# Kernel tuning notes

Hardware: AMD Instinct MI355X
Metric: run time of the kernel (lower is better)

The kernel has to match this reference:

```python
import jax, jax.numpy as jnp
import numpy as np

N_NODES = 50000
N_EDGES = 800000
F_IN = 128
HEADS = 4
C_OUT = 32
NEG_SLOPE = 0.2
BN_EPS = 1e-5


def _add_self_loops(edge_index, edge_attr, n):
    # PyG fill_value='mean': self-loop attr = mean of incoming edge attrs per node (0 if none)
    src, dst = edge_index[0], edge_index[1]
    deg = jax.ops.segment_sum(jnp.ones_like(edge_attr[:, 0]), dst, num_segments=n)
    loop_attr = jax.ops.segment_sum(edge_attr, dst, num_segments=n) / jnp.maximum(deg, 1.0)[:, None]
    loop = jnp.arange(n)
    src2 = jnp.concatenate([src, loop])
    dst2 = jnp.concatenate([dst, loop])
    attr2 = jnp.concatenate([edge_attr, loop_attr], axis=0)
    return src2, dst2, attr2


def _segment_softmax(logits, seg, n):
    m = jax.ops.segment_max(logits, seg, num_segments=n)
    m = jnp.where(jnp.isfinite(m), m, 0.0)
    ex = jnp.exp(logits - m[seg])
    s = jax.ops.segment_sum(ex, seg, num_segments=n)
    return ex / s[seg]


def _gatv2(x, src, dst, eattr, Wl, bl, Wr, br, We, att, bias, n):
    # x: [n, F]; returns [n, HEADS*C_OUT]
    xl = (x @ Wl + bl).reshape(n, HEADS, C_OUT)
    xr = (x @ Wr + br).reshape(n, HEADS, C_OUT)
    ea = (eattr @ We).reshape(-1, HEADS, C_OUT)
    xlj = xl[src]                                   # [E, H, C] gather
    msg = jax.nn.leaky_relu(xlj + xr[dst] + ea, NEG_SLOPE)
    logits = jnp.einsum('ehc,hc->eh', msg, att)     # [E, H]
    alpha = _segment_softmax(logits, dst, n)
    out = jax.ops.segment_sum(xlj * alpha[..., None], dst, num_segments=n)
    return out.reshape(n, HEADS * C_OUT) + bias


def _batchnorm(x, gamma, beta):
    mu = x.mean(axis=0)
    var = x.var(axis=0)
    return gamma * (x - mu) * jax.lax.rsqrt(var + BN_EPS) + beta


def setup_inputs() -> dict:
    key = jax.random.key(0)
    ks = jax.random.split(key, 20)
    HC = HEADS * C_OUT
    s = 0.05
    inp = {
        'emb': jax.random.normal(ks[0], (N_NODES, F_IN), dtype=jnp.float32),
        'edge_index': jax.random.randint(ks[1], (2, N_EDGES), 0, N_NODES, dtype=jnp.int64),
        'edge_weight': jax.random.uniform(ks[2], (N_EDGES, 1), dtype=jnp.float32),
        'Wl1': jax.random.normal(ks[3], (F_IN, HC)) * s,
        'bl1': jnp.zeros((HC,), jnp.float32),
        'Wr1': jax.random.normal(ks[4], (F_IN, HC)) * s,
        'br1': jnp.zeros((HC,), jnp.float32),
        'We1': jax.random.normal(ks[5], (1, HC)) * s,
        'att1': jax.random.normal(ks[6], (HEADS, C_OUT)) * s,
        'bias1': jnp.zeros((HC,), jnp.float32),
        'gamma1': jnp.ones((HC,), jnp.float32),
        'beta1': jnp.zeros((HC,), jnp.float32),
        'Wl2': jax.random.normal(ks[7], (HC, HC)) * s,
        'bl2': jnp.zeros((HC,), jnp.float32),
        'Wr2': jax.random.normal(ks[8], (HC, HC)) * s,
        'br2': jnp.zeros((HC,), jnp.float32),
        'We2': jax.random.normal(ks[9], (1, HC)) * s,
        'att2': jax.random.normal(ks[10], (HEADS, C_OUT)) * s,
        'bias2': jnp.zeros((HC,), jnp.float32),
    }
    return inp


def reference(emb, edge_index, edge_weight, Wl1, bl1, Wr1, br1, We1, att1, bias1,
              gamma1, beta1, Wl2, bl2, Wr2, br2, We2, att2, bias2):
    n = emb.shape[0]
    src, dst, eattr = _add_self_loops(edge_index, edge_weight, n)
    h1 = _gatv2(emb, src, dst, eattr, Wl1, bl1, Wr1, br1, We1, att1, bias1, n)
    h1 = jax.nn.elu(_batchnorm(h1, gamma1, beta1))
    h2 = _gatv2(h1, src, dst, eattr, Wl2, bl2, Wr2, br2, We2, att2, bias2, n)
    # fusion: mean over [input_emb, h1, h2] along stacked axis
    return (emb + h1 + h2) / 3.0
```

## Files before the change

kernel.cpp:

```cpp
#include <hip/hip_runtime.h>
#include <hip/hip_bf16.h>
#include <math.h>

#define N_NODES 50000
#define N_EDGES 800000
#define HC 128
#define SLOT 64

#define BM 128
#define NBX ((N_NODES + BM - 1) / BM)
#define NBKT 64
#define EPB (N_EDGES / NBKT)
#define NW (N_NODES / 2)

typedef short bh8 __attribute__((ext_vector_type(8)));
typedef float f4 __attribute__((ext_vector_type(4)));
typedef float f2 __attribute__((ext_vector_type(2)));

__device__ __forceinline__ unsigned int pk2(float a, float b) {
  return (unsigned int)__bfloat16_as_ushort(__float2bfloat16(a)) |
         ((unsigned int)__bfloat16_as_ushort(__float2bfloat16(b)) << 16);
}
__device__ __forceinline__ float blo(unsigned int u) { return __uint_as_float(u << 16); }
__device__ __forceinline__ float bhi(unsigned int u) { return __uint_as_float(u & 0xffff0000u); }

__global__ __launch_bounds__(256) void k_wprep(
    const float* __restrict__ Wl1, const float* __restrict__ Wr1,
    const float* __restrict__ Wl2, const float* __restrict__ Wr2,
    unsigned short* __restrict__ WtAll,
    float* __restrict__ chsum, float* __restrict__ chsq) {
  int gid = blockIdx.x * 256 + threadIdx.x;
  int m = gid >> 14;
  int idx = gid & 16383;
  const float* src = (m == 0) ? Wl1 : (m == 1) ? Wr1 : (m == 2) ? Wl2 : Wr2;
  int k = idx >> 7, n = idx & 127;
  WtAll[((size_t)m * HC + n) * HC + k] =
      __bfloat16_as_ushort(__float2bfloat16(src[k * HC + n]));
  if (gid < HC) { chsum[gid] = 0.f; chsq[gid] = 0.f; }
}

__global__ __launch_bounds__(1024) void k_hist(const int* __restrict__ ei,
                                               unsigned int* __restrict__ counts32) {
  __shared__ unsigned int hist[NW];
  int tid = threadIdx.x, b = blockIdx.x;
  for (int w = tid; w < NW; w += 1024) hist[w] = 0u;
  __syncthreads();
  const int* dstp = ei + N_EDGES + b * EPB;
  for (int g = tid; g < EPB / 4; g += 1024) {
    int4 d4 = *(const int4*)(dstp + g * 4);
    atomicAdd(&hist[d4.x >> 1], (d4.x & 1) ? 0x10000u : 1u);
    atomicAdd(&hist[d4.y >> 1], (d4.y & 1) ? 0x10000u : 1u);
    atomicAdd(&hist[d4.z >> 1], (d4.z & 1) ? 0x10000u : 1u);
    atomicAdd(&hist[d4.w >> 1], (d4.w & 1) ? 0x10000u : 1u);
  }
  __syncthreads();
  unsigned int* dst = counts32 + (size_t)b * NW;
  for (int w = tid; w < NW; w += 1024) dst[w] = hist[w];
}

__global__ __launch_bounds__(256) void k_scan(const unsigned int* __restrict__ counts32,
                                              unsigned int* __restrict__ bases32,
                                              int* __restrict__ cursor) {
  int w = blockIdx.x * 256 + threadIdx.x;
  if (w >= NW) return;
  unsigned int a0 = 0, a1 = 0;
#pragma unroll 4
  for (int b = 0; b < NBKT; ++b) {
    unsigned int v = counts32[(size_t)b * NW + w];
    bases32[(size_t)b * NW + w] = a0 | (a1 << 16);
    a0 += v & 0xffffu;
    a1 += v >> 16;
  }
  cursor[2 * w] = (int)a0;
  cursor[2 * w + 1] = (int)a1;
}

__global__ __launch_bounds__(256) void k_scat_g1(
    const int* __restrict__ ei, const float* __restrict__ ew,
    const unsigned int* __restrict__ bases32, unsigned int* __restrict__ slots,
    const float* __restrict__ X, const unsigned short* __restrict__ Wt,
    const float* __restrict__ b0, const float* __restrict__ b1,
    unsigned short* __restrict__ Y0b, float* __restrict__ Y1) {
  __shared__ __align__(16) unsigned int lsbuf[NW];
  int tid = threadIdx.x, bid = blockIdx.x;
  if (bid < NBKT) {
    const unsigned int* bp = bases32 + (size_t)bid * NW;
    for (int w = tid; w < NW; w += 256) lsbuf[w] = bp[w];
    __syncthreads();
    const int* sp = ei + bid * EPB;
    const int* dp = ei + N_EDGES + bid * EPB;
    const float* wp = ew + bid * EPB;
    for (int g = tid; g < EPB / 4; g += 256) {
      int4 s4 = *(const int4*)(sp + g * 4);
      int4 d4 = *(const int4*)(dp + g * 4);
      float4 w4 = *(const float4*)(wp + g * 4);
      int ss[4] = {s4.x, s4.y, s4.z, s4.w};
      int dd[4] = {d4.x, d4.y, d4.z, d4.w};
      float ww[4] = {w4.x, w4.y, w4.z, w4.w};
#pragma unroll
      for (int i = 0; i < 4; ++i) {
        unsigned int old = atomicAdd(&lsbuf[dd[i] >> 1], (dd[i] & 1) ? 0x10000u : 1u);
        unsigned int pos = (dd[i] & 1) ? (old >> 16) : (old & 0xffffu);
        unsigned int wq = min((unsigned int)(ww[i] * 65536.f + 0.5f), 65535u);
        if (pos < SLOT)
          slots[(size_t)dd[i] * SLOT + pos] = ((unsigned int)ss[i] << 16) | wq;
      }
    }
    return;
  }
  unsigned short* Xls = (unsigned short*)lsbuf;
  unsigned short* Wls = Xls + 128 * 128;
  int row0 = (bid - NBKT) * BM;
  {
    int r = tid >> 1;
    int ks = (tid & 1) * 64;
    int gr = row0 + r;
    const float* xp = X + (size_t)gr * HC + ks;
    int sw = r & 15;
#pragma unroll
    for (int i = 0; i < 4; ++i) {
      float f[16];
      if (gr < N_NODES) {
        *(float4*)&f[0] = *(const float4*)(xp + i * 16);
        *(float4*)&f[4] = *(const float4*)(xp + i * 16 + 4);
        *(float4*)&f[8] = *(const float4*)(xp + i * 16 + 8);
        *(float4*)&f[12] = *(const float4*)(xp + i * 16 + 12);
      } else {
#pragma unroll
        for (int j = 0; j < 16; ++j) f[j] = 0.f;
      }
      int kg = (ks >> 3) + i * 2;
      *(uint4*)&Xls[r * 128 + ((kg ^ sw) * 8)] =
          make_uint4(pk2(f[0], f[1]), pk2(f[2], f[3]), pk2(f[4], f[5]), pk2(f[6], f[7]));
      *(uint4*)&Xls[r * 128 + (((kg + 1) ^ sw) * 8)] =
          make_uint4(pk2(f[8], f[9]), pk2(f[10], f[11]), pk2(f[12], f[13]), pk2(f[14], f[15]));
    }
  }
  int lane = tid & 63;
  int wv = tid >> 6;
  int lrow = lane & 15;
  int lq = lane >> 4;
  int rbase = wv * 32;
#pragma unroll
  for (int half = 0; half < 2; ++half) {
    if (half) __syncthreads();
    {
      int n = tid >> 1;
      int ks2 = (tid & 1) * 64;
      const unsigned short* wp = Wt + half * (HC * HC) + n * HC + ks2;
      int swn = n & 15;
#pragma unroll
      for (int g = 0; g < 8; ++g) {
        uint4 v = *(const uint4*)(wp + g * 8);
        int kg = (ks2 >> 3) + g;
        *(uint4*)&Wls[n * 128 + ((kg ^ swn) * 8)] = v;
      }
    }
    __syncthreads();
    f4 acc[2][8];
#pragma unroll
    for (int mt = 0; mt < 2; ++mt)
#pragma unroll
      for (int nt = 0; nt < 8; ++nt) acc[mt][nt] = (f4){0.f, 0.f, 0.f, 0.f};
#pragma unroll
    for (int kk = 0; kk < 4; ++kk) {
      int kg = kk * 4 + lq;
      bh8 a0 = *(const bh8*)&Xls[(rbase + lrow) * 128 + ((kg ^ lrow) * 8)];
      bh8 a1 = *(const bh8*)&Xls[(rbase + 16 + lrow) * 128 + ((kg ^ lrow) * 8)];
#pragma unroll
      for (int nt = 0; nt < 8; ++nt) {
        bh8 b = *(const bh8*)&Wls[(nt * 16 + lrow) * 128 + ((kg ^ lrow) * 8)];
        acc[0][nt] = __builtin_amdgcn_mfma_f32_16x16x32_bf16(a0, b, acc[0][nt], 0, 0, 0);
        acc[1][nt] = __builtin_amdgcn_mfma_f32_16x16x32_bf16(a1, b, acc[1][nt], 0, 0, 0);
      }
    }
    const float* bb = half ? b1 : b0;
    float bv[8];
#pragma unroll
    for (int nt = 0; nt < 8; ++nt) bv[nt] = bb[nt * 16 + lrow];
#pragma unroll
    for (int mt = 0; mt < 2; ++mt) {
#pragma unroll
      for (int rr = 0; rr < 4; ++rr) {
        int gr = row0 + rbase + mt * 16 + lq * 4 + rr;
        if (gr < N_NODES) {
          if (half == 0) {
#pragma unroll
            for (int nt = 0; nt < 8; ++nt)
              Y0b[(size_t)gr * HC + nt * 16 + lrow] =
                  __bfloat16_as_ushort(__float2bfloat16(acc[mt][nt][rr] + bv[nt]));
          } else {
#pragma unroll
            for (int nt = 0; nt < 8; ++nt)
              Y1[(size_t)gr * HC + nt * 16 + lrow] = acc[mt][nt][rr] + bv[nt];
          }
        }
      }
    }
  }
}

__global__ __launch_bounds__(256) void k_gemm2(
    const unsigned short* __restrict__ Xb, const unsigned short* __restrict__ Wt,
    const float* __restrict__ b0, const float* __restrict__ b1,
    unsigned char* __restrict__ Y0f8, float* __restrict__ Y1,
    const float* __restrict__ chsum, const float* __restrict__ chsq,
    const float* __restrict__ gamma, const float* __restrict__ beta) {
  __shared__ __align__(16) unsigned short Xls[128 * 128];
  __shared__ __align__(16) unsigned short Wls[128 * 128];
  __shared__ float ssc[HC], ssh[HC];
  int tid = threadIdx.x;
  if (tid < HC) {
    float mu = chsum[tid] * (1.f / N_NODES);
    float var = chsq[tid] * (1.f / N_NODES) - mu * mu;
    float sc = gamma[tid] * rsqrtf(var + 1e-5f);
    ssc[tid] = sc;
    ssh[tid] = beta[tid] - mu * sc;
  }
  __syncthreads();
  int row0 = blockIdx.x * BM;
  {
    int r = tid >> 1;
    int ks = (tid & 1) * 64;
    int gr = row0 + r;
    const unsigned short* xp = Xb + (size_t)gr * HC + ks;
    int sw = r & 15;
#pragma unroll
    for (int i = 0; i < 4; ++i) {
      float f[16];
      if (gr < N_NODES) {
        uint4 ua = *(const uint4*)(xp + i * 16);
        uint4 ub = *(const uint4*)(xp + i * 16 + 8);
        f[0] = blo(ua.x); f[1] = bhi(ua.x); f[2] = blo(ua.y); f[3] = bhi(ua.y);
        f[4] = blo(ua.z); f[5] = bhi(ua.z); f[6] = blo(ua.w); f[7] = bhi(ua.w);
        f[8] = blo(ub.x); f[9] = bhi(ub.x); f[10] = blo(ub.y); f[11] = bhi(ub.y);
        f[12] = blo(ub.z); f[13] = bhi(ub.z); f[14] = blo(ub.w); f[15] = bhi(ub.w);
      } else {
#pragma unroll
        for (int j = 0; j < 16; ++j) f[j] = 0.f;
      }
#pragma unroll
      for (int j = 0; j < 16; ++j) {
        float y = fmaf(f[j], ssc[ks + i * 16 + j], ssh[ks + i * 16 + j]);
        f[j] = (y > 0.f) ? y : (__expf(y) - 1.f);
      }
      int kg = (ks >> 3) + i * 2;
      *(uint4*)&Xls[r * 128 + ((kg ^ sw) * 8)] =
          make_uint4(pk2(f[0], f[1]), pk2(f[2], f[3]), pk2(f[4], f[5]), pk2(f[6], f[7]));
      *(uint4*)&Xls[r * 128 + (((kg + 1) ^ sw) * 8)] =
          make_uint4(pk2(f[8], f[9]), pk2(f[10], f[11]), pk2(f[12], f[13]), pk2(f[14], f[15]));
    }
  }
  int lane = tid & 63;
  int wv = tid >> 6;
  int lrow = lane & 15;
  int lq = lane >> 4;
  int rbase = wv * 32;
#pragma unroll
  for (int half = 0; half < 2; ++half) {
    if (half) __syncthreads();
    {
      int n = tid >> 1;
      int ks = (tid & 1) * 64;
      const unsigned short* wp = Wt + half * (HC * HC) + n * HC + ks;
      int swn = n & 15;
#pragma unroll
      for (int g = 0; g < 8; ++g) {
        uint4 v = *(const uint4*)(wp + g * 8);
        int kg = (ks >> 3) + g;
        *(uint4*)&Wls[n * 128 + ((kg ^ swn) * 8)] = v;
      }
    }
    __syncthreads();
    f4 acc[2][8];
#pragma unroll
    for (int mt = 0; mt < 2; ++mt)
#pragma unroll
      for (int nt = 0; nt < 8; ++nt) acc[mt][nt] = (f4){0.f, 0.f, 0.f, 0.f};
#pragma unroll
    for (int kk = 0; kk < 4; ++kk) {
      int kg = kk * 4 + lq;
      bh8 a0 = *(const bh8*)&Xls[(rbase + lrow) * 128 + ((kg ^ lrow) * 8)];
      bh8 a1 = *(const bh8*)&Xls[(rbase + 16 + lrow) * 128 + ((kg ^ lrow) * 8)];
#pragma unroll
      for (int nt = 0; nt < 8; ++nt) {
        bh8 b = *(const bh8*)&Wls[(nt * 16 + lrow) * 128 + ((kg ^ lrow) * 8)];
        acc[0][nt] = __builtin_amdgcn_mfma_f32_16x16x32_bf16(a0, b, acc[0][nt], 0, 0, 0);
        acc[1][nt] = __builtin_amdgcn_mfma_f32_16x16x32_bf16(a1, b, acc[1][nt], 0, 0, 0);
      }
    }
    const float* bb = half ? b1 : b0;
    float bv[8];
#pragma unroll
    for (int nt = 0; nt < 8; ++nt) bv[nt] = bb[nt * 16 + lrow];
#pragma unroll
    for (int mt = 0; mt < 2; ++mt) {
#pragma unroll
      for (int rr = 0; rr < 4; ++rr) {
        int gr = row0 + rbase + mt * 16 + lq * 4 + rr;
        if (gr < N_NODES) {
          if (half == 0) {
#pragma unroll
            for (int nt = 0; nt < 8; ++nt) {
              float v = acc[mt][nt][rr] + bv[nt];
              int p = __builtin_amdgcn_cvt_pk_fp8_f32(v, v, 0, false);
              Y0f8[(size_t)gr * HC + nt * 16 + lrow] = (unsigned char)(p & 0xff);
            }
          } else {
#pragma unroll
            for (int nt = 0; nt < 8; ++nt)
              Y1[(size_t)gr * HC + nt * 16 + lrow] = acc[mt][nt][rr] + bv[nt];
          }
        }
      }
    }
  }
}

template <int FINAL, int F8>
__global__ __launch_bounds__(256) void k_gat(
    const void* __restrict__ xlv, const float* __restrict__ xr,
    const int* __restrict__ cursor, const unsigned int* __restrict__ slots,
    const float* __restrict__ We, const float* __restrict__ att,
    const float* __restrict__ bias, void* __restrict__ out,
    const float* __restrict__ emb, const unsigned short* __restrict__ h1p,
    const float* __restrict__ chsum, const float* __restrict__ chsq,
    const float* __restrict__ gamma, const float* __restrict__ beta) {
  int g = threadIdx.x >> 5;
  int lane = threadIdx.x & 31;
  int n = blockIdx.x * 8 + g;
  int fi = n * 32 + lane;
  const uint2* xl2 = (const uint2*)xlv;
  const unsigned int* xf = (const unsigned int*)xlv;
  float4 xr4 = ((const float4*)xr)[fi];
  float4 we4 = ((const float4*)We)[lane];
  float4 at4 = ((const float4*)att)[lane];
  int deg = min(cursor[n], SLOT);
  int base = n * SLOT;
  int deg32 = min(deg, 32);

  unsigned int ev = (lane < deg32) ? slots[base + lane] : 0u;
  float evw = (float)(ev & 0xffffu) * (1.f / 65536.f);
  float wsum = evw;
#pragma unroll
  for (int m = 16; m >= 1; m >>= 1) wsum += __shfl_xor(wsum, m);

  float l = 0.f;
  float4 o = make_float4(0.f, 0.f, 0.f, 0.f);

  auto decode = [&](uint2 gc) -> float4 {
    float4 xlj;
    if (F8) {
      f2 ab = __builtin_amdgcn_cvt_pk_f32_fp8((int)gc.x, false);
      f2 cd = __builtin_amdgcn_cvt_pk_f32_fp8((int)gc.x, true);
      xlj.x = ab[0]; xlj.y = ab[1]; xlj.z = cd[0]; xlj.w = cd[1];
    } else {
      xlj.x = blo(gc.x); xlj.y = bhi(gc.x);
      xlj.z = blo(gc.y); xlj.w = bhi(gc.y);
    }
    return xlj;
  };
  auto edge_body = [&](float w, uint2 gc, bool valid) {
    float4 xlj = decode(gc);
    float4 v;
    v.x = fmaf(w, we4.x, xlj.x + xr4.x);
    v.y = fmaf(w, we4.y, xlj.y + xr4.y);
    v.z = fmaf(w, we4.z, xlj.z + xr4.z);
    v.w = fmaf(w, we4.w, xlj.w + xr4.w);
    v.x = fmaxf(v.x, 0.2f * v.x);
    v.y = fmaxf(v.y, 0.2f * v.y);
    v.z = fmaxf(v.z, 0.2f * v.z);
    v.w = fmaxf(v.w, 0.2f * v.w);
    float p = v.x * at4.x + v.y * at4.y + v.z * at4.z + v.w * at4.w;
    p += __shfl_xor(p, 1);
    p += __shfl_xor(p, 2);
    p += __shfl_xor(p, 4);
    float e = valid ? __expf(p) : 0.f;
    l += e;
    o.x = fmaf(e, xlj.x, o.x);
    o.y = fmaf(e, xlj.y, o.y);
    o.z = fmaf(e, xlj.z, o.z);
    o.w = fmaf(e, xlj.w, o.w);
  };
  auto fetch = [&](int j, uint2& qq, float& ww) {
    int jc = min(j, deg32 - 1);
    unsigned int evj = __shfl(ev, jc, 32);
    ww = (float)(evj & 0xffffu) * (1.f / 65536.f);
    int s = (int)(evj >> 16);
    if (F8) qq.x = xf[s * 32 + lane];
    else qq = xl2[s * 32 + lane];
  };

  if (deg32 > 0) {
    uint2 q0, q1, q2, q3;
    float w0, w1, w2, w3;
    fetch(0, q0, w0);
    fetch(1, q1, w1);
    fetch(2, q2, w2);
    fetch(3, q3, w3);
    for (int b = 0; b < deg32; b += 4) {
      uint2 c0 = q0, c1 = q1, c2 = q2, c3 = q3;
      float x0 = w0, x1 = w1, x2 = w2, x3 = w3;
      fetch(b + 4, q0, w0);
      fetch(b + 5, q1, w1);
      fetch(b + 6, q2, w2);
      fetch(b + 7, q3, w3);
      edge_body(x0, c0, true);
      edge_body(x1, c1, b + 1 < deg32);
      edge_body(x2, c2, b + 2 < deg32);
      edge_body(x3, c3, b + 3 < deg32);
    }
  }
  if (deg > 32) {
    for (int j = base + 32; j < base + deg; ++j) {
      unsigned int evj = slots[j];
      float w = (float)(evj & 0xffffu) * (1.f / 65536.f);
      wsum += w;
      int s = (int)(evj >> 16);
      uint2 gc;
      if (F8) gc.x = xf[s * 32 + lane];
      else gc = xl2[s * 32 + lane];
      edge_body(w, gc, true);
    }
  }
  {
    float wself = (deg > 0) ? wsum / (float)deg : 0.f;
    uint2 gs;
    if (F8) gs.x = xf[n * 32 + lane];
    else gs = xl2[n * 32 + lane];
    edge_body(wself, gs, true);
  }

  float inv = 1.f / l;
  float4 b4 = ((const float4*)bias)[lane];
  float4 r;
  r.x = fmaf(o.x, inv, b4.x);
  r.y = fmaf(o.y, inv, b4.y);
  r.z = fmaf(o.z, inv, b4.z);
  r.w = fmaf(o.w, inv, b4.w);
  if (FINAL) {
    float4 e4 = ((const float4*)emb)[fi];
    uint2 hh = ((const uint2*)h1p)[fi];
    float4 h4;
    h4.x = blo(hh.x); h4.y = bhi(hh.x); h4.z = blo(hh.y); h4.w = bhi(hh.y);
    float4 cs = ((const float4*)chsum)[lane];
    float4 cq = ((const float4*)chsq)[lane];
    float4 gm = ((const float4*)gamma)[lane];
    float4 bt = ((const float4*)beta)[lane];
    const float invN = 1.f / N_NODES;
    float4 sc4, sh4;
    {
      float mu = cs.x * invN, var = cq.x * invN - mu * mu;
      sc4.x = gm.x * rsqrtf(var + 1e-5f); sh4.x = bt.x - mu * sc4.x;
      mu = cs.y * invN; var = cq.y * invN - mu * mu;
      sc4.y = gm.y * rsqrtf(var + 1e-5f); sh4.y = bt.y - mu * sc4.y;
      mu = cs.z * invN; var = cq.z * invN - mu * mu;
      sc4.z = gm.z * rsqrtf(var + 1e-5f); sh4.z = bt.z - mu * sc4.z;
      mu = cs.w * invN; var = cq.w * invN - mu * mu;
      sc4.w = gm.w * rsqrtf(var + 1e-5f); sh4.w = bt.w - mu * sc4.w;
    }
    float4 h;
    h.x = fmaf(h4.x, sc4.x, sh4.x);
    h.y = fmaf(h4.y, sc4.y, sh4.y);
    h.z = fmaf(h4.z, sc4.z, sh4.z);
    h.w = fmaf(h4.w, sc4.w, sh4.w);
    h.x = (h.x > 0.f) ? h.x : (__expf(h.x) - 1.f);
    h.y = (h.y > 0.f) ? h.y : (__expf(h.y) - 1.f);
    h.z = (h.z > 0.f) ? h.z : (__expf(h.z) - 1.f);
    h.w = (h.w > 0.f) ? h.w : (__expf(h.w) - 1.f);
    const float k3 = 1.f / 3.f;
    r.x = (e4.x + h.x + r.x) * k3;
    r.y = (e4.y + h.y + r.y) * k3;
    r.z = (e4.z + h.z + r.z) * k3;
    r.w = (e4.w + h.w + r.w) * k3;
    ((float4*)out)[fi] = r;
  } else {
    ((uint2*)out)[fi] = make_uint2(pk2(r.x, r.y), pk2(r.z, r.w));
  }
}

#define BN_ROWS 200
__global__ __launch_bounds__(256) void k_bnstats(const unsigned short* __restrict__ h1b,
                                                 float* __restrict__ chsum,
                                                 float* __restrict__ chsq) {
  int c2 = threadIdx.x & 63;
  int g = threadIdx.x >> 6;
  int r0 = blockIdx.x * BN_ROWS;
  float s0 = 0.f, s1 = 0.f, q0 = 0.f, q1 = 0.f;
  const unsigned int* h32 = (const unsigned int*)h1b;
  for (int r = r0 + g; r < r0 + BN_ROWS; r += 4) {
    unsigned int u = h32[(size_t)r * 64 + c2];
    float a = blo(u), b = bhi(u);
    s0 += a; q0 += a * a;
    s1 += b; q1 += b * b;
  }
  __shared__ float sh[256][4];
  sh[threadIdx.x][0] = s0; sh[threadIdx.x][1] = q0;
  sh[threadIdx.x][2] = s1; sh[threadIdx.x][3] = q1;
  __syncthreads();
  if (g == 0) {
    float ts0 = 0.f, tq0 = 0.f, ts1 = 0.f, tq1 = 0.f;
#pragma unroll
    for (int gg = 0; gg < 4; ++gg) {
      ts0 += sh[gg * 64 + c2][0]; tq0 += sh[gg * 64 + c2][1];
      ts1 += sh[gg * 64 + c2][2]; tq1 += sh[gg * 64 + c2][3];
    }
    atomicAdd(chsum + 2 * c2, ts0);
    atomicAdd(chsq + 2 * c2, tq0);
    atomicAdd(chsum + 2 * c2 + 1, ts1);
    atomicAdd(chsq + 2 * c2 + 1, tq1);
  }
}

extern "C" void kernel_launch(void* const* d_in, const int* in_sizes, int n_in,
                              void* d_out, int out_size, void* d_ws, size_t ws_size,
                              hipStream_t stream) {
  const float* emb = (const float*)d_in[0];
  const int* ei = (const int*)d_in[1];
  const float* ew = (const float*)d_in[2];
  const float* Wl1 = (const float*)d_in[3];
  const float* bl1 = (const float*)d_in[4];
  const float* Wr1 = (const float*)d_in[5];
  const float* br1 = (const float*)d_in[6];
  const float* We1 = (const float*)d_in[7];
  const float* att1 = (const float*)d_in[8];
  const float* bias1 = (const float*)d_in[9];
  const float* gamma1 = (const float*)d_in[10];
  const float* beta1 = (const float*)d_in[11];
  const float* Wl2 = (const float*)d_in[12];
  const float* bl2 = (const float*)d_in[13];
  const float* Wr2 = (const float*)d_in[14];
  const float* br2 = (const float*)d_in[15];
  const float* We2 = (const float*)d_in[16];
  const float* att2 = (const float*)d_in[17];
  const float* bias2 = (const float*)d_in[18];
  float* out = (float*)d_out;

  char* wsb = (char*)d_ws;
  size_t off = 0;
  auto alloc = [&](size_t bytes) -> void* {
    void* p = (void*)(wsb + off);
    off += (bytes + 255) & ~(size_t)255;
    return p;
  };
  int* cursor = (int*)alloc((size_t)N_NODES * 4);
  float* chsum = (float*)alloc(HC * 4);
  float* chsq = (float*)alloc(HC * 4);
  unsigned short* WtAll = (unsigned short*)alloc((size_t)4 * HC * HC * 2);
  unsigned int* counts32 = (unsigned int*)alloc((size_t)NBKT * NW * 4);
  unsigned int* bases32 = (unsigned int*)alloc((size_t)NBKT * NW * 4);
  unsigned int* slots = (unsigned int*)alloc((size_t)N_NODES * SLOT * 4);
  unsigned short* xlb = (unsigned short*)alloc((size_t)N_NODES * HC * 2);
  unsigned char* xlf8 = (unsigned char*)alloc((size_t)N_NODES * HC);
  float* xr = (float*)alloc((size_t)N_NODES * HC * 4);
  unsigned short* h1b = (unsigned short*)alloc((size_t)N_NODES * HC * 2);

  k_wprep<<<256, 256, 0, stream>>>(Wl1, Wr1, Wl2, Wr2, WtAll, chsum, chsq);
  k_hist<<<NBKT, 1024, 0, stream>>>(ei, counts32);
  k_scan<<<(NW + 255) / 256, 256, 0, stream>>>(counts32, bases32, cursor);
  k_scat_g1<<<NBKT + NBX, 256, 0, stream>>>(ei, ew, bases32, slots, emb, WtAll,
                                            bl1, br1, xlb, xr);
  k_gat<0, 0><<<N_NODES / 8, 256, 0, stream>>>(xlb, xr, cursor, slots, We1, att1,
                                               bias1, (void*)h1b, nullptr, nullptr,
                                               nullptr, nullptr, nullptr, nullptr);
  k_bnstats<<<N_NODES / BN_ROWS, 256, 0, stream>>>(h1b, chsum, chsq);
  k_gemm2<<<NBX, 256, 0, stream>>>(h1b, WtAll + 2 * HC * HC, bl2, br2, xlf8, xr,
                                   chsum, chsq, gamma1, beta1);
  k_gat<1, 1><<<N_NODES / 8, 256, 0, stream>>>(xlf8, xr, cursor, slots, We2, att2,
                                               bias2, (void*)out, emb, h1b,
                                               chsum, chsq, gamma1, beta1);
}
```

Before: 278.5 us.

## Split histogram and scatter blocks by node range, fuse weight prep into histogram

Each edge chunk is now handled by four blocks, each owning a quarter of the destination node range, so the per-block LDS histogram shrinks to 25 KB instead of 100 KB. This should allow higher occupancy and more blocks in flight for both the histogram and the scatter phases. The weight transpose/prep is merged into the histogram kernel, removing one launch. The cost is that each block reads the full edge chunk, so edge-index traffic is four times higher, with most edges filtered out.

```diff
diff --git a/kernel.cpp b/kernel.cpp
--- a/kernel.cpp
+++ b/kernel.cpp
@@ -9,9 +9,13 @@
 
 #define BM 128
 #define NBX ((N_NODES + BM - 1) / BM)
-#define NBKT 64
-#define EPB (N_EDGES / NBKT)
+#define NCHK 64
+#define EPB (N_EDGES / NCHK)
+#define NRNG 4
+#define RNG_N (N_NODES / NRNG)
+#define RNG_W (RNG_N / 2)
 #define NW (N_NODES / 2)
+#define NSCAT (NCHK * NRNG)
 
 typedef short bh8 __attribute__((ext_vector_type(8)));
 typedef float f4 __attribute__((ext_vector_type(4)));
@@ -24,38 +28,40 @@
 __device__ __forceinline__ float blo(unsigned int u) { return __uint_as_float(u << 16); }
 __device__ __forceinline__ float bhi(unsigned int u) { return __uint_as_float(u & 0xffff0000u); }
 
-__global__ __launch_bounds__(256) void k_wprep(
+__global__ __launch_bounds__(256) void k_histprep(
     const float* __restrict__ Wl1, const float* __restrict__ Wr1,
     const float* __restrict__ Wl2, const float* __restrict__ Wr2,
     unsigned short* __restrict__ WtAll,
-    float* __restrict__ chsum, float* __restrict__ chsq) {
-  int gid = blockIdx.x * 256 + threadIdx.x;
-  int m = gid >> 14;
-  int idx = gid & 16383;
-  const float* src = (m == 0) ? Wl1 : (m == 1) ? Wr1 : (m == 2) ? Wl2 : Wr2;
-  int k = idx >> 7, n = idx & 127;
-  WtAll[((size_t)m * HC + n) * HC + k] =
-      __bfloat16_as_ushort(__float2bfloat16(src[k * HC + n]));
-  if (gid < HC) { chsum[gid] = 0.f; chsq[gid] = 0.f; }
-}
-
-__global__ __launch_bounds__(1024) void k_hist(const int* __restrict__ ei,
-                                               unsigned int* __restrict__ counts32) {
-  __shared__ unsigned int hist[NW];
-  int tid = threadIdx.x, b = blockIdx.x;
-  for (int w = tid; w < NW; w += 1024) hist[w] = 0u;
+    float* __restrict__ chsum, float* __restrict__ chsq,
+    const int* __restrict__ ei, unsigned int* __restrict__ counts32) {
+  __shared__ unsigned int hist[RNG_W];
+  int tid = threadIdx.x, bid = blockIdx.x;
+  int gid = bid * 256 + tid;
+  {
+    int m = gid >> 14;
+    int idx = gid & 16383;
+    const float* src = (m == 0) ? Wl1 : (m == 1) ? Wr1 : (m == 2) ? Wl2 : Wr2;
+    int k = idx >> 7, n = idx & 127;
+    WtAll[((size_t)m * HC + n) * HC + k] =
+        __bfloat16_as_ushort(__float2bfloat16(src[k * HC + n]));
+    if (gid < HC) { chsum[gid] = 0.f; chsq[gid] = 0.f; }
+  }
+  int c = bid >> 2, r = bid & 3;
+  int rb = r * RNG_N;
+  for (int w = tid; w < RNG_W; w += 256) hist[w] = 0u;
   __syncthreads();
-  const int* dstp = ei + N_EDGES + b * EPB;
-  for (int g = tid; g < EPB / 4; g += 1024) {
+  const int* dstp = ei + N_EDGES + c * EPB;
+  for (int g = tid; g < EPB / 4; g += 256) {
     int4 d4 = *(const int4*)(dstp + g * 4);
-    atomicAdd(&hist[d4.x >> 1], (d4.x & 1) ? 0x10000u : 1u);
-    atomicAdd(&hist[d4.y >> 1], (d4.y & 1) ? 0x10000u : 1u);
-    atomicAdd(&hist[d4.z >> 1], (d4.z & 1) ? 0x10000u : 1u);
-    atomicAdd(&hist[d4.w >> 1], (d4.w & 1) ? 0x10000u : 1u);
+    int dl;
+    dl = d4.x - rb; if ((unsigned)dl < RNG_N) atomicAdd(&hist[dl >> 1], (dl & 1) ? 0x10000u : 1u);
+    dl = d4.y - rb; if ((unsigned)dl < RNG_N) atomicAdd(&hist[dl >> 1], (dl & 1) ? 0x10000u : 1u);
+    dl = d4.z - rb; if ((unsigned)dl < RNG_N) atomicAdd(&hist[dl >> 1], (dl & 1) ? 0x10000u : 1u);
+    dl = d4.w - rb; if ((unsigned)dl < RNG_N) atomicAdd(&hist[dl >> 1], (dl & 1) ? 0x10000u : 1u);
   }
   __syncthreads();
-  unsigned int* dst = counts32 + (size_t)b * NW;
-  for (int w = tid; w < NW; w += 1024) dst[w] = hist[w];
+  unsigned int* dst = counts32 + (size_t)c * NW + r * RNG_W;
+  for (int w = tid; w < RNG_W; w += 256) dst[w] = hist[w];
 }
 
 __global__ __launch_bounds__(256) void k_scan(const unsigned int* __restrict__ counts32,
@@ -65,7 +71,7 @@
   if (w >= NW) return;
   unsigned int a0 = 0, a1 = 0;
 #pragma unroll 4
-  for (int b = 0; b < NBKT; ++b) {
+  for (int b = 0; b < NCHK; ++b) {
     unsigned int v = counts32[(size_t)b * NW + w];
     bases32[(size_t)b * NW + w] = a0 | (a1 << 16);
     a0 += v & 0xffffu;
@@ -81,15 +87,17 @@
     const float* __restrict__ X, const unsigned short* __restrict__ Wt,
     const float* __restrict__ b0, const float* __restrict__ b1,
     unsigned short* __restrict__ Y0b, float* __restrict__ Y1) {
-  __shared__ __align__(16) unsigned int lsbuf[NW];
+  __shared__ __align__(16) unsigned int lsbuf[16384];
   int tid = threadIdx.x, bid = blockIdx.x;
-  if (bid < NBKT) {
-    const unsigned int* bp = bases32 + (size_t)bid * NW;
-    for (int w = tid; w < NW; w += 256) lsbuf[w] = bp[w];
+  if (bid < NSCAT) {
+    int c = bid >> 2, r = bid & 3;
+    int rb = r * RNG_N;
+    const unsigned int* bp = bases32 + (size_t)c * NW + r * RNG_W;
+    for (int w = tid; w < RNG_W; w += 256) lsbuf[w] = bp[w];
     __syncthreads();
-    const int* sp = ei + bid * EPB;
-    const int* dp = ei + N_EDGES + bid * EPB;
-    const float* wp = ew + bid * EPB;
+    const int* sp = ei + c * EPB;
+    const int* dp = ei + N_EDGES + c * EPB;
+    const float* wp = ew + c * EPB;
     for (int g = tid; g < EPB / 4; g += 256) {
       int4 s4 = *(const int4*)(sp + g * 4);
       int4 d4 = *(const int4*)(dp + g * 4);
@@ -99,18 +107,21 @@
       float ww[4] = {w4.x, w4.y, w4.z, w4.w};
 #pragma unroll
       for (int i = 0; i < 4; ++i) {
-        unsigned int old = atomicAdd(&lsbuf[dd[i] >> 1], (dd[i] & 1) ? 0x10000u : 1u);
-        unsigned int pos = (dd[i] & 1) ? (old >> 16) : (old & 0xffffu);
-        unsigned int wq = min((unsigned int)(ww[i] * 65536.f + 0.5f), 65535u);
-        if (pos < SLOT)
-          slots[(size_t)dd[i] * SLOT + pos] = ((unsigned int)ss[i] << 16) | wq;
+        int dl = dd[i] - rb;
+        if ((unsigned)dl < RNG_N) {
+          unsigned int old = atomicAdd(&lsbuf[dl >> 1], (dl & 1) ? 0x10000u : 1u);
+          unsigned int pos = (dl & 1) ? (old >> 16) : (old & 0xffffu);
+          unsigned int wq = min((unsigned int)(ww[i] * 65536.f + 0.5f), 65535u);
+          if (pos < SLOT)
+            slots[(size_t)dd[i] * SLOT + pos] = ((unsigned int)ss[i] << 16) | wq;
+        }
       }
     }
     return;
   }
   unsigned short* Xls = (unsigned short*)lsbuf;
   unsigned short* Wls = Xls + 128 * 128;
-  int row0 = (bid - NBKT) * BM;
+  int row0 = (bid - NSCAT) * BM;
   {
     int r = tid >> 1;
     int ks = (tid & 1) * 64;
@@ -547,19 +558,19 @@
   float* chsum = (float*)alloc(HC * 4);
   float* chsq = (float*)alloc(HC * 4);
   unsigned short* WtAll = (unsigned short*)alloc((size_t)4 * HC * HC * 2);
-  unsigned int* counts32 = (unsigned int*)alloc((size_t)NBKT * NW * 4);
-  unsigned int* bases32 = (unsigned int*)alloc((size_t)NBKT * NW * 4);
+  unsigned int* counts32 = (unsigned int*)alloc((size_t)NCHK * NW * 4);
+  unsigned int* bases32 = (unsigned int*)alloc((size_t)NCHK * NW * 4);
   unsigned int* slots = (unsigned int*)alloc((size_t)N_NODES * SLOT * 4);
   unsigned short* xlb = (unsigned short*)alloc((size_t)N_NODES * HC * 2);
   unsigned char* xlf8 = (unsigned char*)alloc((size_t)N_NODES * HC);
   float* xr = (float*)alloc((size_t)N_NODES * HC * 4);
   unsigned short* h1b = (unsigned short*)alloc((size_t)N_NODES * HC * 2);
 
-  k_wprep<<<256, 256, 0, stream>>>(Wl1, Wr1, Wl2, Wr2, WtAll, chsum, chsq);
-  k_hist<<<NBKT, 1024, 0, stream>>>(ei, counts32);
+  k_histprep<<<NSCAT, 256, 0, stream>>>(Wl1, Wr1, Wl2, Wr2, WtAll, chsum, chsq,
+                                        ei, counts32);
   k_scan<<<(NW + 255) / 256, 256, 0, stream>>>(counts32, bases32, cursor);
-  k_scat_g1<<<NBKT + NBX, 256, 0, stream>>>(ei, ew, bases32, slots, emb, WtAll,
-                                            bl1, br1, xlb, xr);
+  k_scat_g1<<<NSCAT + NBX, 256, 0, stream>>>(ei, ew, bases32, slots, emb, WtAll,
+                                             bl1, br1, xlb, xr);
   k_gat<0, 0><<<N_NODES / 8, 256, 0, stream>>>(xlb, xr, cursor, slots, We1, att1,
                                                bias1, (void*)h1b, nullptr, nullptr,
                                                nullptr, nullptr, nullptr, nullptr);
```

After: 285.9 us. 1.03x slower.
